# Performance work log

Measured on AMD Instinct MI355X. Metric: run time of the kernel, lower is better.

The kernel has to match this reference:

```python
import jax, jax.numpy as jnp
import numpy as np

IN_DIM, HID, OUT_DIM, PRED_LEN = 33, 64, 2, 25
B, P, T = 1024, 22, 20
EPS = 1e-5


def _lstm_step(Wih, Whh, b, h, c, xt):
    # PyTorch gate order: i, f, g, o
    gates = xt @ Wih.T + h @ Whh.T + b
    i, f, g, o = jnp.split(gates, 4, axis=-1)
    c_new = jax.nn.sigmoid(f) * c + jax.nn.sigmoid(i) * jnp.tanh(g)
    h_new = jax.nn.sigmoid(o) * jnp.tanh(c_new)
    return h_new, c_new


def setup_inputs() -> dict:
    key = jax.random.key(0)
    ks = jax.random.split(key, 20)
    s = 0.1
    inp = {
        "x": jax.random.normal(ks[0], (B, P, T, IN_DIM), dtype=jnp.float32),
        "enc_Wih": jax.random.normal(ks[1], (4 * HID, IN_DIM)) * s,
        "enc_Whh": jax.random.normal(ks[2], (4 * HID, HID)) * s,
        "enc_bih": jax.random.normal(ks[3], (4 * HID,)) * s,
        "enc_bhh": jax.random.normal(ks[4], (4 * HID,)) * s,
        "q_W": jax.random.normal(ks[5], (HID, HID)) * s,
        "q_b": jax.random.normal(ks[6], (HID,)) * s,
        "k_W": jax.random.normal(ks[7], (HID, HID)) * s,
        "k_b": jax.random.normal(ks[8], (HID,)) * s,
        "v_W": jax.random.normal(ks[9], (HID, HID)) * s,
        "v_b": jax.random.normal(ks[10], (HID,)) * s,
        "ln_g": jnp.ones((HID,), jnp.float32),
        "ln_b": jnp.zeros((HID,), jnp.float32),
        "dec_Wih": jax.random.normal(ks[11], (4 * HID, OUT_DIM)) * s,
        "dec_Whh": jax.random.normal(ks[12], (4 * HID, HID)) * s,
        "dec_bih": jax.random.normal(ks[13], (4 * HID,)) * s,
        "dec_bhh": jax.random.normal(ks[14], (4 * HID,)) * s,
        "fc_W": jax.random.normal(ks[15], (OUT_DIM, HID)) * s,
        "fc_b": jax.random.normal(ks[16], (OUT_DIM,)) * s,
    }
    return inp


def reference(x, enc_Wih, enc_Whh, enc_bih, enc_bhh, q_W, q_b, k_W, k_b,
              v_W, v_b, ln_g, ln_b, dec_Wih, dec_Whh, dec_bih, dec_bhh,
              fc_W, fc_b):
    b, p, t, d = x.shape
    n = b * p
    xf = x.reshape(n, t, d)

    # ----- encoder LSTM over history -----
    b_enc = enc_bih + enc_bhh
    def enc_step(carry, xt):
        h, c = carry
        h, c = _lstm_step(enc_Wih, enc_Whh, b_enc, h, c, xt)
        return (h, c), None
    h0 = jnp.zeros((n, HID), x.dtype)
    (hn, cn), _ = jax.lax.scan(enc_step, (h0, h0), xf.transpose(1, 0, 2))

    # ----- interaction GNN (self-attention over players) -----
    last_hidden = hn.reshape(b, p, HID)
    Q = last_hidden @ q_W.T + q_b
    K = last_hidden @ k_W.T + k_b
    V = last_hidden @ v_W.T + v_b
    scores = jnp.einsum('bph,bqh->bpq', Q, K) / jnp.sqrt(jnp.float32(HID))
    attn = jax.nn.softmax(scores, axis=-1)
    ctx = jnp.einsum('bpq,bqh->bph', attn, V)

    # ----- layernorm(residual) -----
    y = last_hidden + ctx
    mu = y.mean(-1, keepdims=True)
    var = y.var(-1, keepdims=True)
    y = (y - mu) / jnp.sqrt(var + EPS) * ln_g + ln_b

    b_dec = dec_bih + dec_bhh
    def dec_step(carry, _):
        h, c, inp = carry
        h, c = _lstm_step(dec_Wih, dec_Whh, b_dec, h, c, inp)
        pred = h @ fc_W.T + fc_b
        return (h, c, pred), pred
    inp0 = xf[:, -1, :OUT_DIM]
    _, preds = jax.lax.scan(dec_step, (y.reshape(n, HID), cn, inp0),
                            None, length=PRED_LEN)  # [PRED_LEN, n, 2]
    return preds.transpose(1, 0, 2).reshape(b, p, PRED_LEN, OUT_DIM)
```

## Files before the change

kernel.cpp:

```cpp
#include <hip/hip_runtime.h>

typedef short short8 __attribute__((ext_vector_type(8)));
typedef float f32x4 __attribute__((ext_vector_type(4)));

#define IN_DIM   33
#define HID      64
#define OUT_DIM  2
#define PRED_LEN 25
#define NB       1024
#define NP       22
#define NT       20
#define EPS      1e-5f

#define SWZ(s,k) (((s) << 7) + ((k) ^ (((s) & 7) << 3)))

__device__ __forceinline__ float fast_rcp(float x){ return __builtin_amdgcn_rcpf(x); }
__device__ __forceinline__ float sigm(float x){ return fast_rcp(1.0f + __expf(-x)); }
__device__ __forceinline__ float tanhf_(float x){ float e = __expf(2.0f*x); return 1.0f - 2.0f*fast_rcp(e + 1.0f); }
__device__ __forceinline__ unsigned short bf_hi(float f){
    unsigned u = __float_as_uint(f);
    return (unsigned short)((u + 0x7fffu + ((u >> 16) & 1u)) >> 16);
}
__device__ __forceinline__ float bf_f(unsigned short h){ return __uint_as_float(((unsigned)h) << 16); }
__device__ __forceinline__ unsigned cvt_pk_bf16(float a, float b){
    unsigned r;
    asm("v_cvt_pk_bf16_f32 %0, %1, %2" : "=v"(r) : "v"(a), "v"(b));
    return r;
}

__global__ __launch_bounds__(256, 2) void nfl_mfma(
    const float* __restrict__ x,
    const float* __restrict__ enc_Wih, const float* __restrict__ enc_Whh,
    const float* __restrict__ enc_bih, const float* __restrict__ enc_bhh,
    const float* __restrict__ q_W, const float* __restrict__ q_b,
    const float* __restrict__ k_W, const float* __restrict__ k_b,
    const float* __restrict__ v_W, const float* __restrict__ v_b,
    const float* __restrict__ ln_g, const float* __restrict__ ln_b,
    const float* __restrict__ dec_Wih, const float* __restrict__ dec_Whh,
    const float* __restrict__ dec_bih, const float* __restrict__ dec_bhh,
    const float* __restrict__ fc_W, const float* __restrict__ fc_b,
    float* __restrict__ out)
{
    __shared__ __align__(16) unsigned char arena[4*8192];
    __shared__ float sh_q [NP*66];
    __shared__ float sh_f [NP*66];
    __shared__ float sh_sc[NP*24];
    __shared__ float sh_p0[32];
    __shared__ float sh_p1[32];
    __shared__ float sh_mu[NP];
    __shared__ float sh_rs[NP];

    float* sh_k = (float*)(arena + 16384);
    float* sh_v = (float*)(arena + 16384 + 8192);

    const int tid  = threadIdx.x;
    const int w    = tid >> 6;
    const int ln   = tid & 63;
    const int lo15 = ln & 15;
    const int qq   = ln >> 4;
    const int jh   = 16*w + lo15;
    const int b    = blockIdx.x;
    const float* xb = x + (size_t)b * NP*NT*IN_DIM;

    auto Ahi = [&](int p){ return (unsigned short*)(arena + p*16384); };
    auto Alo = [&](int p){ return (unsigned short*)(arena + p*16384 + 8192); };

    short8 eBh[4][4], eBl[4][4];
    float bias_e[4];
    #pragma unroll
    for (int nt = 0; nt < 4; nt++){
        int g = 16*w + 64*nt + lo15;
        bias_e[nt] = enc_bih[g] + enc_bhh[g];
        #pragma unroll
        for (int kt = 0; kt < 4; kt++){
            #pragma unroll
            for (int e = 0; e < 8; e++){
                int k = 32*kt + 8*qq + e;
                float v;
                if (k < HID) v = enc_Whh[g*HID + k];
                else { int d = k - HID; v = (d < IN_DIM) ? enc_Wih[g*IN_DIM + d] : 0.0f; }
                unsigned short h = bf_hi(v);
                eBh[nt][kt][e] = (short)h;
                eBl[nt][kt][e] = (short)bf_hi(v - bf_f(h));
            }
        }
    }

    for (int i = tid; i < 4*2048; i += 256) ((unsigned*)arena)[i] = 0;

    float cst[2][4] = {{0,0,0,0},{0,0,0,0}};
    __syncthreads();

    auto nonlin_store = [&](f32x4 (&acc)[2][4], unsigned short* wh,
                            unsigned short* wl, bool save_f){
        #pragma unroll
        for (int m = 0; m < 2; m++){
            #pragma unroll
            for (int jp = 0; jp < 2; jp++){
                const int j0 = 2*jp;
                float hh0, hh1;
                {
                    float gi=acc[m][0][j0], gf=acc[m][1][j0], gg=acc[m][2][j0], go=acc[m][3][j0];
                    float c = sigm(gf)*cst[m][j0] + sigm(gi)*tanhf_(gg);
                    cst[m][j0] = c;
                    hh0 = sigm(go)*tanhf_(c);
                }
                {
                    float gi=acc[m][0][j0+1], gf=acc[m][1][j0+1], gg=acc[m][2][j0+1], go=acc[m][3][j0+1];
                    float c = sigm(gf)*cst[m][j0+1] + sigm(gi)*tanhf_(gg);
                    cst[m][j0+1] = c;
                    hh1 = sigm(go)*tanhf_(c);
                }
                unsigned hp = cvt_pk_bf16(hh0, hh1);
                float r0 = hh0 - __uint_as_float(hp << 16);
                float r1 = hh1 - __uint_as_float(hp & 0xffff0000u);
                unsigned lp = cvt_pk_bf16(r0, r1);
                const int s0 = 16*m + 4*qq + j0;
                if (s0 < NP){
                    int i0 = SWZ(s0, jh);
                    wh[i0] = (unsigned short)hp;
                    wl[i0] = (unsigned short)lp;
                    if (save_f) sh_f[s0*66 + jh] = hh0;
                }
                if (s0 + 1 < NP){
                    int i1 = SWZ(s0 + 1, jh);
                    wh[i1] = (unsigned short)(hp >> 16);
                    wl[i1] = (unsigned short)(lp >> 16);
                    if (save_f) sh_f[(s0+1)*66 + jh] = hh1;
                }
            }
        }
    };

    {
        unsigned short* wh = Ahi(0); unsigned short* wl = Alo(0);
        for (int i = tid; i < NP*IN_DIM; i += 256){
            int s = i / IN_DIM, d = i - s * IN_DIM;
            float v = xb[(s*NT + 0)*IN_DIM + d];
            unsigned short h = bf_hi(v);
            int idx = SWZ(s, HID + d);
            wh[idx] = h; wl[idx] = bf_hi(v - bf_f(h));
        }
    }
    __syncthreads();

    for (int t = 0; t < NT; t++){
        const int p = t & 1;
        unsigned short* rh = Ahi(p);     unsigned short* rl = Alo(p);
        unsigned short* wh = Ahi(1 - p); unsigned short* wl = Alo(1 - p);

        float xr[3];
        const bool have_x = (t + 1 < NT);
        if (have_x){
            #pragma unroll
            for (int sl = 0; sl < 3; sl++){
                int i = tid + 256*sl;
                if (i < NP*IN_DIM){
                    int s = i / IN_DIM, d = i - s * IN_DIM;
                    xr[sl] = xb[(s*NT + (t+1))*IN_DIM + d];
                }
            }
        }

        f32x4 acc[2][4];
        #pragma unroll
        for (int m = 0; m < 2; m++)
            #pragma unroll
            for (int nt = 0; nt < 4; nt++){
                float bb = bias_e[nt];
                acc[m][nt][0]=bb; acc[m][nt][1]=bb; acc[m][nt][2]=bb; acc[m][nt][3]=bb;
            }
        #pragma unroll
        for (int kt = 0; kt < 4; kt++){
            #pragma unroll
            for (int m = 0; m < 2; m++){
                int idx = SWZ(16*m + lo15, 32*kt + 8*qq);
                short8 ah = *reinterpret_cast<const short8*>(&rh[idx]);
                short8 al = *reinterpret_cast<const short8*>(&rl[idx]);
                #pragma unroll
                for (int nt = 0; nt < 4; nt++){
                    acc[m][nt] = __builtin_amdgcn_mfma_f32_16x16x32_bf16(ah, eBh[nt][kt], acc[m][nt], 0,0,0);
                    acc[m][nt] = __builtin_amdgcn_mfma_f32_16x16x32_bf16(al, eBh[nt][kt], acc[m][nt], 0,0,0);
                    acc[m][nt] = __builtin_amdgcn_mfma_f32_16x16x32_bf16(ah, eBl[nt][kt], acc[m][nt], 0,0,0);
                }
            }
        }
        nonlin_store(acc, wh, wl, t == NT-1);
        if (have_x){
            #pragma unroll
            for (int sl = 0; sl < 3; sl++){
                int i = tid + 256*sl;
                if (i < NP*IN_DIM){
                    int s = i / IN_DIM, d = i - s * IN_DIM;
                    unsigned short h = bf_hi(xr[sl]);
                    int idx = SWZ(s, HID + d);
                    wh[idx] = h; wl[idx] = bf_hi(xr[sl] - bf_f(h));
                }
            }
        }
        __syncthreads();
    }

    {
        unsigned short* rh = Ahi(0); unsigned short* rl = Alo(0);
        short8 qBh[3][2], qBl[3][2];
        float qb3[3];
        #pragma unroll
        for (int mat = 0; mat < 3; mat++){
            const float* W  = (mat==0) ? q_W : (mat==1) ? k_W : v_W;
            const float* bb = (mat==0) ? q_b : (mat==1) ? k_b : v_b;
            qb3[mat] = bb[jh];
            #pragma unroll
            for (int kt = 0; kt < 2; kt++){
                #pragma unroll
                for (int e = 0; e < 8; e++){
                    int k = 32*kt + 8*qq + e;
                    float v = W[jh*HID + k];
                    unsigned short h = bf_hi(v);
                    qBh[mat][kt][e] = (short)h;
                    qBl[mat][kt][e] = (short)bf_hi(v - bf_f(h));
                }
            }
        }
        f32x4 qacc[3][2];
        #pragma unroll
        for (int mat = 0; mat < 3; mat++)
            #pragma unroll
            for (int m = 0; m < 2; m++){
                float bb = qb3[mat];
                qacc[mat][m][0]=bb; qacc[mat][m][1]=bb; qacc[mat][m][2]=bb; qacc[mat][m][3]=bb;
            }
        #pragma unroll
        for (int kt = 0; kt < 2; kt++){
            #pragma unroll
            for (int m = 0; m < 2; m++){
                int idx = SWZ(16*m + lo15, 32*kt + 8*qq);
                short8 ah = *reinterpret_cast<const short8*>(&rh[idx]);
                short8 al = *reinterpret_cast<const short8*>(&rl[idx]);
                #pragma unroll
                for (int mat = 0; mat < 3; mat++){
                    qacc[mat][m] = __builtin_amdgcn_mfma_f32_16x16x32_bf16(ah, qBh[mat][kt], qacc[mat][m], 0,0,0);
                    qacc[mat][m] = __builtin_amdgcn_mfma_f32_16x16x32_bf16(al, qBh[mat][kt], qacc[mat][m], 0,0,0);
                    qacc[mat][m] = __builtin_amdgcn_mfma_f32_16x16x32_bf16(ah, qBl[mat][kt], qacc[mat][m], 0,0,0);
                }
            }
        }
        #pragma unroll
        for (int mat = 0; mat < 3; mat++){
            float* dst = (mat==0) ? sh_q : (mat==1) ? sh_k : sh_v;
            #pragma unroll
            for (int m = 0; m < 2; m++)
                #pragma unroll
                for (int j = 0; j < 4; j++){
                    int s = 16*m + 4*qq + j;
                    if (s < NP) dst[s*66 + jh] = qacc[mat][m][j];
                }
        }
    }
    __syncthreads();

    for (int i = tid; i < NP*NP; i += 256){
        int p = i / NP, q = i - p*NP;
        float acc = 0.0f;
        #pragma unroll
        for (int k = 0; k < HID; k++) acc = fmaf(sh_q[p*66 + k], sh_k[q*66 + k], acc);
        sh_sc[p*24 + q] = acc * 0.125f;
    }
    __syncthreads();

    if (tid < NP){
        float m = -1e30f;
        for (int q = 0; q < NP; q++) m = fmaxf(m, sh_sc[tid*24 + q]);
        float sum = 0.0f;
        for (int q = 0; q < NP; q++){ float e = __expf(sh_sc[tid*24 + q] - m); sh_sc[tid*24 + q] = e; sum += e; }
        float inv = fast_rcp(sum);
        for (int q = 0; q < NP; q++) sh_sc[tid*24 + q] *= inv;
    }
    __syncthreads();

    for (int i = tid; i < NP*HID; i += 256){
        int s = i >> 6, j = i & 63;
        float acc = 0.0f;
        #pragma unroll
        for (int q = 0; q < NP; q++) acc = fmaf(sh_sc[s*24 + q], sh_v[q*66 + j], acc);
        sh_f[s*66 + j] += acc;
    }
    __syncthreads();

    if (tid < NP){
        float mu = 0.0f;
        for (int j = 0; j < HID; j++) mu += sh_f[tid*66 + j];
        mu *= (1.0f/HID);
        float var = 0.0f;
        for (int j = 0; j < HID; j++){ float d = sh_f[tid*66 + j] - mu; var += d*d; }
        sh_mu[tid] = mu;
        sh_rs[tid] = rsqrtf(var*(1.0f/HID) + EPS);
    }
    __syncthreads();

    {
        unsigned short* wh = Ahi(0); unsigned short* wl = Alo(0);
        for (int i = tid; i < NP*HID/2; i += 256){
            int s = i >> 5, j0 = (i & 31) << 1;
            float sc = sh_rs[s], mu = sh_mu[s];
            float v0 = (sh_f[s*66 + j0]   - mu) * sc * ln_g[j0]   + ln_b[j0];
            float v1 = (sh_f[s*66 + j0+1] - mu) * sc * ln_g[j0+1] + ln_b[j0+1];
            unsigned hp = cvt_pk_bf16(v0, v1);
            float r0 = v0 - __uint_as_float(hp << 16);
            float r1 = v1 - __uint_as_float(hp & 0xffff0000u);
            unsigned lp = cvt_pk_bf16(r0, r1);
            int idx = SWZ(s, j0);
            *(unsigned*)&wh[idx] = hp;
            *(unsigned*)&wl[idx] = lp;
        }
    }
    if (tid < 32){
        float v0 = 0.0f, v1 = 0.0f;
        if (tid < NP){
            v0 = xb[(tid*NT + NT-1)*IN_DIM + 0];
            v1 = xb[(tid*NT + NT-1)*IN_DIM + 1];
        }
        sh_p0[tid] = v0; sh_p1[tid] = v1;
    }

    short8 dBh[4][2], dBl[4][2];
    float bias_d[4], wd0[4], wd1[4];
    #pragma unroll
    for (int nt = 0; nt < 4; nt++){
        int g = 16*w + 64*nt + lo15;
        bias_d[nt] = dec_bih[g] + dec_bhh[g];
        wd0[nt] = dec_Wih[g*OUT_DIM + 0];
        wd1[nt] = dec_Wih[g*OUT_DIM + 1];
        #pragma unroll
        for (int kt = 0; kt < 2; kt++){
            #pragma unroll
            for (int e = 0; e < 8; e++){
                int k = 32*kt + 8*qq + e;
                float v = dec_Whh[g*HID + k];
                unsigned short h = bf_hi(v);
                dBh[nt][kt][e] = (short)h;
                dBl[nt][kt][e] = (short)bf_hi(v - bf_f(h));
            }
        }
    }
    const int fitem = tid >> 2, fq = tid & 3, fs = fitem >> 1, fo = fitem & 1;
    float fcw[16]; float fcb = 0.0f;
    if (tid < 176){
        #pragma unroll
        for (int jj = 0; jj < 16; jj++) fcw[jj] = fc_W[fo*HID + 16*fq + jj];
        fcb = fc_b[fo];
    }
    float* outb = out + (size_t)b * NP * PRED_LEN * OUT_DIM;
    __syncthreads();

    for (int t = 0; t < PRED_LEN; t++){
        const int p = t & 1;
        unsigned short* rh = Ahi(p);     unsigned short* rl = Alo(p);
        unsigned short* wh = Ahi(1 - p); unsigned short* wl = Alo(1 - p);

        f32x4 acc[2][4];
        #pragma unroll
        for (int m = 0; m < 2; m++){
            #pragma unroll
            for (int j = 0; j < 4; j++){
                int s = 16*m + 4*qq + j;
                float p0 = sh_p0[s], p1 = sh_p1[s];
                #pragma unroll
                for (int nt = 0; nt < 4; nt++)
                    acc[m][nt][j] = bias_d[nt] + wd0[nt]*p0 + wd1[nt]*p1;
            }
        }
        #pragma unroll
        for (int kt = 0; kt < 2; kt++){
            #pragma unroll
            for (int m = 0; m < 2; m++){
                int idx = SWZ(16*m + lo15, 32*kt + 8*qq);
                short8 ah = *reinterpret_cast<const short8*>(&rh[idx]);
                short8 al = *reinterpret_cast<const short8*>(&rl[idx]);
                #pragma unroll
                for (int nt = 0; nt < 4; nt++){
                    acc[m][nt] = __builtin_amdgcn_mfma_f32_16x16x32_bf16(ah, dBh[nt][kt], acc[m][nt], 0,0,0);
                    acc[m][nt] = __builtin_amdgcn_mfma_f32_16x16x32_bf16(al, dBh[nt][kt], acc[m][nt], 0,0,0);
                    acc[m][nt] = __builtin_amdgcn_mfma_f32_16x16x32_bf16(ah, dBl[nt][kt], acc[m][nt], 0,0,0);
                }
            }
        }
        nonlin_store(acc, wh, wl, false);
        __syncthreads();

        if (tid < 176){
            int idx0 = SWZ(fs, 16*fq);
            int idx1 = SWZ(fs, 16*fq + 8);
            short8 h0h = *reinterpret_cast<const short8*>(&wh[idx0]);
            short8 h0l = *reinterpret_cast<const short8*>(&wl[idx0]);
            short8 h1h = *reinterpret_cast<const short8*>(&wh[idx1]);
            short8 h1l = *reinterpret_cast<const short8*>(&wl[idx1]);
            float part = 0.0f;
            #pragma unroll
            for (int e = 0; e < 8; e++){
                part = fmaf(bf_f((unsigned short)h0h[e]) + bf_f((unsigned short)h0l[e]), fcw[e],     part);
                part = fmaf(bf_f((unsigned short)h1h[e]) + bf_f((unsigned short)h1l[e]), fcw[8 + e], part);
            }
            part += __shfl_xor(part, 1);
            part += __shfl_xor(part, 2);
            if (fq == 0){
                float pred = part + fcb;
                outb[(fs*PRED_LEN + t)*OUT_DIM + fo] = pred;
                if (fo == 0) sh_p0[fs] = pred; else sh_p1[fs] = pred;
            }
        }
        __syncthreads();
    }
}

extern "C" void kernel_launch(void* const* d_in, const int* in_sizes, int n_in,
                              void* d_out, int out_size, void* d_ws, size_t ws_size,
                              hipStream_t stream) {
    const float* x        = (const float*)d_in[0];
    const float* enc_Wih  = (const float*)d_in[1];
    const float* enc_Whh  = (const float*)d_in[2];
    const float* enc_bih  = (const float*)d_in[3];
    const float* enc_bhh  = (const float*)d_in[4];
    const float* q_W      = (const float*)d_in[5];
    const float* q_b      = (const float*)d_in[6];
    const float* k_W      = (const float*)d_in[7];
    const float* k_b      = (const float*)d_in[8];
    const float* v_W      = (const float*)d_in[9];
    const float* v_b      = (const float*)d_in[10];
    const float* ln_g     = (const float*)d_in[11];
    const float* ln_b     = (const float*)d_in[12];
    const float* dec_Wih  = (const float*)d_in[13];
    const float* dec_Whh  = (const float*)d_in[14];
    const float* dec_bih  = (const float*)d_in[15];
    const float* dec_bhh  = (const float*)d_in[16];
    const float* fc_W     = (const float*)d_in[17];
    const float* fc_b     = (const float*)d_in[18];
    float* out = (float*)d_out;

    nfl_mfma<<<dim3(NB), dim3(256), 0, stream>>>(
        x, enc_Wih, enc_Whh, enc_bih, enc_bhh,
        q_W, q_b, k_W, k_b, v_W, v_b, ln_g, ln_b,
        dec_Wih, dec_Whh, dec_bih, dec_bhh, fc_W, fc_b, out);
}
```

Before: 359.7 us.

## Process two batch groups per block to fill MFMA row tiles

Each block now handles two batches (44 player rows padded to 48) instead of one, using three 16-row MFMA tiles rather than two. The old layout wasted 10 of 32 padded rows, and the new one wastes 4 of 48, so more useful work is done per LSTM step and per barrier. Weight fragments loaded into registers are also shared across twice the rows. The grid is halved to 512 blocks. Shared memory is reorganised to fit, with attention scores, layernorm stats and decoder inputs packed into unused parts of the arena. The trade-offs are more registers, fewer blocks to fill the 256 CUs, and extra index arithmetic.

Measured after the change: 339.6 us. 5.6% less time.

```diff
diff --git a/kernel.cpp b/kernel.cpp
--- a/kernel.cpp
+++ b/kernel.cpp
@@ -11,6 +11,7 @@
 #define NP       22
 #define NT       20
 #define EPS      1e-5f
+#define QSTR     65
 
 #define SWZ(s,k) (((s) << 7) + ((k) ^ (((s) & 7) << 3)))
 
@@ -41,17 +42,12 @@
     const float* __restrict__ fc_W, const float* __restrict__ fc_b,
     float* __restrict__ out)
 {
-    __shared__ __align__(16) unsigned char arena[4*8192];
-    __shared__ float sh_q [NP*66];
-    __shared__ float sh_f [NP*66];
-    __shared__ float sh_sc[NP*24];
-    __shared__ float sh_p0[32];
-    __shared__ float sh_p1[32];
-    __shared__ float sh_mu[NP];
-    __shared__ float sh_rs[NP];
-
-    float* sh_k = (float*)(arena + 16384);
-    float* sh_v = (float*)(arena + 16384 + 8192);
+    __shared__ __align__(16) unsigned char arena[2*24576];
+    __shared__ float sh_q[44*QSTR];
+
+    float* arena_f = (float*)arena;
+    float* sh_k = (float*)(arena + 24576);
+    float* sh_v = sh_k + 44*QSTR;
 
     const int tid  = threadIdx.x;
     const int w    = tid >> 6;
@@ -59,11 +55,12 @@
     const int lo15 = ln & 15;
     const int qq   = ln >> 4;
     const int jh   = 16*w + lo15;
-    const int b    = blockIdx.x;
-    const float* xb = x + (size_t)b * NP*NT*IN_DIM;
-
-    auto Ahi = [&](int p){ return (unsigned short*)(arena + p*16384); };
-    auto Alo = [&](int p){ return (unsigned short*)(arena + p*16384 + 8192); };
+    const int bid  = blockIdx.x;
+    const float* xb0 = x + (size_t)(2*bid) * NP*NT*IN_DIM;
+    const float* xb1 = xb0 + NP*NT*IN_DIM;
+
+    auto Ahi = [&](int p){ return (unsigned short*)(arena + p*24576); };
+    auto Alo = [&](int p){ return (unsigned short*)(arena + p*24576 + 12288); };
 
     short8 eBh[4][4], eBl[4][4];
     float bias_e[4];
@@ -86,61 +83,86 @@
         }
     }
 
-    for (int i = tid; i < 4*2048; i += 256) ((unsigned*)arena)[i] = 0;
-
-    float cst[2][4] = {{0,0,0,0},{0,0,0,0}};
-    __syncthreads();
-
-    auto nonlin_store = [&](f32x4 (&acc)[2][4], unsigned short* wh,
-                            unsigned short* wl, bool save_f){
-        #pragma unroll
-        for (int m = 0; m < 2; m++){
+    for (int i = tid; i < 12288; i += 256) ((unsigned*)arena)[i] = 0;
+
+    float cst[3][4];
+    #pragma unroll
+    for (int mt = 0; mt < 3; mt++)
+        #pragma unroll
+        for (int j = 0; j < 4; j++) cst[mt][j] = 0.0f;
+    __syncthreads();
+
+    auto stage_x_regs = [&](int t, float (&xr)[6]){
+        #pragma unroll
+        for (int sl = 0; sl < 6; sl++){
+            int i = tid + 256*sl;
+            if (i < 2*NP*IN_DIM){
+                int bb = (i >= NP*IN_DIM);
+                int rem = i - bb*NP*IN_DIM;
+                int s = rem / IN_DIM, d = rem - s*IN_DIM;
+                const float* xb = bb ? xb1 : xb0;
+                xr[sl] = xb[(s*NT + t)*IN_DIM + d];
+            }
+        }
+    };
+    auto stage_x_write = [&](float (&xr)[6], unsigned short* wh, unsigned short* wl){
+        #pragma unroll
+        for (int sl = 0; sl < 6; sl++){
+            int i = tid + 256*sl;
+            if (i < 2*NP*IN_DIM){
+                int bb = (i >= NP*IN_DIM);
+                int rem = i - bb*NP*IN_DIM;
+                int s = rem / IN_DIM, d = rem - s*IN_DIM;
+                unsigned short h = bf_hi(xr[sl]);
+                int idx = SWZ(bb*24 + s, HID + d);
+                wh[idx] = h; wl[idx] = bf_hi(xr[sl] - bf_f(h));
+            }
+        }
+    };
+
+    auto nonlin_store = [&](f32x4 (&acc)[3][4], unsigned short* wh, unsigned short* wl){
+        #pragma unroll
+        for (int mt = 0; mt < 3; mt++){
             #pragma unroll
             for (int jp = 0; jp < 2; jp++){
                 const int j0 = 2*jp;
                 float hh0, hh1;
                 {
-                    float gi=acc[m][0][j0], gf=acc[m][1][j0], gg=acc[m][2][j0], go=acc[m][3][j0];
-                    float c = sigm(gf)*cst[m][j0] + sigm(gi)*tanhf_(gg);
-                    cst[m][j0] = c;
+                    float gi=acc[mt][0][j0], gf=acc[mt][1][j0], gg=acc[mt][2][j0], go=acc[mt][3][j0];
+                    float c = sigm(gf)*cst[mt][j0] + sigm(gi)*tanhf_(gg);
+                    cst[mt][j0] = c;
                     hh0 = sigm(go)*tanhf_(c);
                 }
                 {
-                    float gi=acc[m][0][j0+1], gf=acc[m][1][j0+1], gg=acc[m][2][j0+1], go=acc[m][3][j0+1];
-                    float c = sigm(gf)*cst[m][j0+1] + sigm(gi)*tanhf_(gg);
-                    cst[m][j0+1] = c;
+                    float gi=acc[mt][0][j0+1], gf=acc[mt][1][j0+1], gg=acc[mt][2][j0+1], go=acc[mt][3][j0+1];
+                    float c = sigm(gf)*cst[mt][j0+1] + sigm(gi)*tanhf_(gg);
+                    cst[mt][j0+1] = c;
                     hh1 = sigm(go)*tanhf_(c);
                 }
                 unsigned hp = cvt_pk_bf16(hh0, hh1);
                 float r0 = hh0 - __uint_as_float(hp << 16);
                 float r1 = hh1 - __uint_as_float(hp & 0xffff0000u);
                 unsigned lp = cvt_pk_bf16(r0, r1);
-                const int s0 = 16*m + 4*qq + j0;
-                if (s0 < NP){
+                const int s0 = 16*mt + 4*qq + j0;
+                const int ps0 = s0 - ((s0 >= 24) ? 24 : 0);
+                if (ps0 < NP){
                     int i0 = SWZ(s0, jh);
                     wh[i0] = (unsigned short)hp;
                     wl[i0] = (unsigned short)lp;
-                    if (save_f) sh_f[s0*66 + jh] = hh0;
-                }
-                if (s0 + 1 < NP){
+                }
+                if (ps0 + 1 < NP){
                     int i1 = SWZ(s0 + 1, jh);
                     wh[i1] = (unsigned short)(hp >> 16);
                     wl[i1] = (unsigned short)(lp >> 16);
-                    if (save_f) sh_f[(s0+1)*66 + jh] = hh1;
                 }
             }
         }
     };
 
     {
-        unsigned short* wh = Ahi(0); unsigned short* wl = Alo(0);
-        for (int i = tid; i < NP*IN_DIM; i += 256){
-            int s = i / IN_DIM, d = i - s * IN_DIM;
-            float v = xb[(s*NT + 0)*IN_DIM + d];
-            unsigned short h = bf_hi(v);
-            int idx = SWZ(s, HID + d);
-            wh[idx] = h; wl[idx] = bf_hi(v - bf_f(h));
-        }
+        float xr[6];
+        stage_x_regs(0, xr);
+        stage_x_write(xr, Ahi(0), Alo(0));
     }
     __syncthreads();
 
@@ -149,55 +171,35 @@
         unsigned short* rh = Ahi(p);     unsigned short* rl = Alo(p);
         unsigned short* wh = Ahi(1 - p); unsigned short* wl = Alo(1 - p);
 
-        float xr[3];
+        float xr[6];
         const bool have_x = (t + 1 < NT);
-        if (have_x){
-            #pragma unroll
-            for (int sl = 0; sl < 3; sl++){
-                int i = tid + 256*sl;
-                if (i < NP*IN_DIM){
-                    int s = i / IN_DIM, d = i - s * IN_DIM;
-                    xr[sl] = xb[(s*NT + (t+1))*IN_DIM + d];
-                }
-            }
-        }
-
-        f32x4 acc[2][4];
-        #pragma unroll
-        for (int m = 0; m < 2; m++)
+        if (have_x) stage_x_regs(t + 1, xr);
+
+        f32x4 acc[3][4];
+        #pragma unroll
+        for (int mt = 0; mt < 3; mt++)
             #pragma unroll
             for (int nt = 0; nt < 4; nt++){
                 float bb = bias_e[nt];
-                acc[m][nt][0]=bb; acc[m][nt][1]=bb; acc[m][nt][2]=bb; acc[m][nt][3]=bb;
+                acc[mt][nt][0]=bb; acc[mt][nt][1]=bb; acc[mt][nt][2]=bb; acc[mt][nt][3]=bb;
             }
         #pragma unroll
         for (int kt = 0; kt < 4; kt++){
             #pragma unroll
-            for (int m = 0; m < 2; m++){
-                int idx = SWZ(16*m + lo15, 32*kt + 8*qq);
+            for (int mt = 0; mt < 3; mt++){
+                int idx = SWZ(16*mt + lo15, 32*kt + 8*qq);
                 short8 ah = *reinterpret_cast<const short8*>(&rh[idx]);
                 short8 al = *reinterpret_cast<const short8*>(&rl[idx]);
                 #pragma unroll
                 for (int nt = 0; nt < 4; nt++){
-                    acc[m][nt] = __builtin_amdgcn_mfma_f32_16x16x32_bf16(ah, eBh[nt][kt], acc[m][nt], 0,0,0);
-                    acc[m][nt] = __builtin_amdgcn_mfma_f32_16x16x32_bf16(al, eBh[nt][kt], acc[m][nt], 0,0,0);
-                    acc[m][nt] = __builtin_amdgcn_mfma_f32_16x16x32_bf16(ah, eBl[nt][kt], acc[m][nt], 0,0,0);
-                }
-            }
-        }
-        nonlin_store(acc, wh, wl, t == NT-1);
-        if (have_x){
-            #pragma unroll
-            for (int sl = 0; sl < 3; sl++){
-                int i = tid + 256*sl;
-                if (i < NP*IN_DIM){
-                    int s = i / IN_DIM, d = i - s * IN_DIM;
-                    unsigned short h = bf_hi(xr[sl]);
-                    int idx = SWZ(s, HID + d);
-                    wh[idx] = h; wl[idx] = bf_hi(xr[sl] - bf_f(h));
-                }
-            }
-        }
+                    acc[mt][nt] = __builtin_amdgcn_mfma_f32_16x16x32_bf16(ah, eBh[nt][kt], acc[mt][nt], 0,0,0);
+                    acc[mt][nt] = __builtin_amdgcn_mfma_f32_16x16x32_bf16(al, eBh[nt][kt], acc[mt][nt], 0,0,0);
+                    acc[mt][nt] = __builtin_amdgcn_mfma_f32_16x16x32_bf16(ah, eBl[nt][kt], acc[mt][nt], 0,0,0);
+                }
+            }
+        }
+        nonlin_store(acc, wh, wl);
+        if (have_x) stage_x_write(xr, wh, wl);
         __syncthreads();
     }
 
@@ -222,26 +224,26 @@
                 }
             }
         }
-        f32x4 qacc[3][2];
+        f32x4 qacc[3][3];
         #pragma unroll
         for (int mat = 0; mat < 3; mat++)
             #pragma unroll
-            for (int m = 0; m < 2; m++){
+            for (int mt = 0; mt < 3; mt++){
                 float bb = qb3[mat];
-                qacc[mat][m][0]=bb; qacc[mat][m][1]=bb; qacc[mat][m][2]=bb; qacc[mat][m][3]=bb;
+                qacc[mat][mt][0]=bb; qacc[mat][mt][1]=bb; qacc[mat][mt][2]=bb; qacc[mat][mt][3]=bb;
             }
         #pragma unroll
         for (int kt = 0; kt < 2; kt++){
             #pragma unroll
-            for (int m = 0; m < 2; m++){
-                int idx = SWZ(16*m + lo15, 32*kt + 8*qq);
+            for (int mt = 0; mt < 3; mt++){
+                int idx = SWZ(16*mt + lo15, 32*kt + 8*qq);
                 short8 ah = *reinterpret_cast<const short8*>(&rh[idx]);
                 short8 al = *reinterpret_cast<const short8*>(&rl[idx]);
                 #pragma unroll
                 for (int mat = 0; mat < 3; mat++){
-                    qacc[mat][m] = __builtin_amdgcn_mfma_f32_16x16x32_bf16(ah, qBh[mat][kt], qacc[mat][m], 0,0,0);
-                    qacc[mat][m] = __builtin_amdgcn_mfma_f32_16x16x32_bf16(al, qBh[mat][kt], qacc[mat][m], 0,0,0);
-                    qacc[mat][m] = __builtin_amdgcn_mfma_f32_16x16x32_bf16(ah, qBl[mat][kt], qacc[mat][m], 0,0,0);
+                    qacc[mat][mt] = __builtin_amdgcn_mfma_f32_16x16x32_bf16(ah, qBh[mat][kt], qacc[mat][mt], 0,0,0);
+                    qacc[mat][mt] = __builtin_amdgcn_mfma_f32_16x16x32_bf16(al, qBh[mat][kt], qacc[mat][mt], 0,0,0);
+                    qacc[mat][mt] = __builtin_amdgcn_mfma_f32_16x16x32_bf16(ah, qBl[mat][kt], qacc[mat][mt], 0,0,0);
                 }
             }
         }
@@ -249,78 +251,107 @@
         for (int mat = 0; mat < 3; mat++){
             float* dst = (mat==0) ? sh_q : (mat==1) ? sh_k : sh_v;
             #pragma unroll
-            for (int m = 0; m < 2; m++)
+            for (int mt = 0; mt < 3; mt++)
                 #pragma unroll
                 for (int j = 0; j < 4; j++){
-                    int s = 16*m + 4*qq + j;
-                    if (s < NP) dst[s*66 + jh] = qacc[mat][m][j];
-                }
-        }
-    }
-    __syncthreads();
-
-    for (int i = tid; i < NP*NP; i += 256){
-        int p = i / NP, q = i - p*NP;
+                    int s = 16*mt + 4*qq + j;
+                    int bb = (s >= 24) ? 1 : 0;
+                    int ps = s - 24*bb;
+                    if (ps < NP) dst[(bb*NP + ps)*QSTR + jh] = qacc[mat][mt][j];
+                }
+        }
+    }
+    __syncthreads();
+
+    for (int i = tid; i < 2*NP*NP; i += 256){
+        int bb = (i >= NP*NP);
+        int rem = i - bb*NP*NP;
+        int p = rem / NP, q = rem - p*NP;
         float acc = 0.0f;
         #pragma unroll
-        for (int k = 0; k < HID; k++) acc = fmaf(sh_q[p*66 + k], sh_k[q*66 + k], acc);
-        sh_sc[p*24 + q] = acc * 0.125f;
-    }
-    __syncthreads();
-
-    if (tid < NP){
+        for (int k = 0; k < HID; k++)
+            acc = fmaf(sh_q[(bb*NP + p)*QSTR + k], sh_k[(bb*NP + q)*QSTR + k], acc);
+        arena_f[(bb*24 + p)*64 + 32 + q] = acc * 0.125f;
+    }
+    __syncthreads();
+
+    if (tid < 2*NP){
+        int bb = (tid >= NP);
+        int p = tid - bb*NP;
+        float* row = arena_f + (bb*24 + p)*64 + 32;
         float m = -1e30f;
-        for (int q = 0; q < NP; q++) m = fmaxf(m, sh_sc[tid*24 + q]);
+        for (int q = 0; q < NP; q++) m = fmaxf(m, row[q]);
         float sum = 0.0f;
-        for (int q = 0; q < NP; q++){ float e = __expf(sh_sc[tid*24 + q] - m); sh_sc[tid*24 + q] = e; sum += e; }
+        for (int q = 0; q < NP; q++){ float e = __expf(row[q] - m); row[q] = e; sum += e; }
         float inv = fast_rcp(sum);
-        for (int q = 0; q < NP; q++) sh_sc[tid*24 + q] *= inv;
-    }
-    __syncthreads();
-
-    for (int i = tid; i < NP*HID; i += 256){
-        int s = i >> 6, j = i & 63;
-        float acc = 0.0f;
-        #pragma unroll
-        for (int q = 0; q < NP; q++) acc = fmaf(sh_sc[s*24 + q], sh_v[q*66 + j], acc);
-        sh_f[s*66 + j] += acc;
-    }
-    __syncthreads();
-
-    if (tid < NP){
+        for (int q = 0; q < NP; q++) row[q] *= inv;
+    }
+    __syncthreads();
+
+    {
+        unsigned short* h0 = Ahi(0); unsigned short* l0 = Alo(0);
+        for (int i = tid; i < 2*NP*HID; i += 256){
+            int bb = (i >= NP*HID);
+            int rem = i - bb*NP*HID;
+            int ps = rem >> 6, j = rem & 63;
+            int r = bb*24 + ps;
+            const float* sc = arena_f + r*64 + 32;
+            float acc = 0.0f;
+            #pragma unroll
+            for (int q = 0; q < NP; q++) acc = fmaf(sc[q], sh_v[(bb*NP + q)*QSTR + j], acc);
+            int idx = SWZ(r, j);
+            float h = bf_f(h0[idx]) + bf_f(l0[idx]);
+            sh_q[(bb*NP + ps)*QSTR + j] = h + acc;
+        }
+    }
+    __syncthreads();
+
+    if (tid < 2*NP){
+        int bb = (tid >= NP);
+        int ps = tid - bb*NP;
+        const float* yrow = sh_q + (bb*NP + ps)*QSTR;
         float mu = 0.0f;
-        for (int j = 0; j < HID; j++) mu += sh_f[tid*66 + j];
+        for (int j = 0; j < HID; j++) mu += yrow[j];
         mu *= (1.0f/HID);
         float var = 0.0f;
-        for (int j = 0; j < HID; j++){ float d = sh_f[tid*66 + j] - mu; var += d*d; }
-        sh_mu[tid] = mu;
-        sh_rs[tid] = rsqrtf(var*(1.0f/HID) + EPS);
+        for (int j = 0; j < HID; j++){ float d = yrow[j] - mu; var += d*d; }
+        arena_f[(bb*24 + ps)*64 + 32 + 22] = mu;
+        arena_f[(bb*24 + ps)*64 + 32 + 23] = rsqrtf(var*(1.0f/HID) + EPS);
     }
     __syncthreads();
 
     {
         unsigned short* wh = Ahi(0); unsigned short* wl = Alo(0);
-        for (int i = tid; i < NP*HID/2; i += 256){
-            int s = i >> 5, j0 = (i & 31) << 1;
-            float sc = sh_rs[s], mu = sh_mu[s];
-            float v0 = (sh_f[s*66 + j0]   - mu) * sc * ln_g[j0]   + ln_b[j0];
-            float v1 = (sh_f[s*66 + j0+1] - mu) * sc * ln_g[j0+1] + ln_b[j0+1];
+        for (int i = tid; i < 2*NP*HID/2; i += 256){
+            int bb = (i >= NP*HID/2);
+            int rem = i - bb*NP*HID/2;
+            int ps = rem >> 5, j0 = (rem & 31) << 1;
+            int r = bb*24 + ps;
+            float mu = arena_f[r*64 + 32 + 22];
+            float sc = arena_f[r*64 + 32 + 23];
+            const float* yrow = sh_q + (bb*NP + ps)*QSTR;
+            float v0 = (yrow[j0]   - mu) * sc * ln_g[j0]   + ln_b[j0];
+            float v1 = (yrow[j0+1] - mu) * sc * ln_g[j0+1] + ln_b[j0+1];
             unsigned hp = cvt_pk_bf16(v0, v1);
             float r0 = v0 - __uint_as_float(hp << 16);
             float r1 = v1 - __uint_as_float(hp & 0xffff0000u);
             unsigned lp = cvt_pk_bf16(r0, r1);
-            int idx = SWZ(s, j0);
+            int idx = SWZ(r, j0);
             *(unsigned*)&wh[idx] = hp;
             *(unsigned*)&wl[idx] = lp;
         }
     }
-    if (tid < 32){
+    if (tid < 48){
+        int bb = (tid >= 24);
+        int ps = tid - 24*bb;
         float v0 = 0.0f, v1 = 0.0f;
-        if (tid < NP){
-            v0 = xb[(tid*NT + NT-1)*IN_DIM + 0];
-            v1 = xb[(tid*NT + NT-1)*IN_DIM + 1];
-        }
-        sh_p0[tid] = v0; sh_p1[tid] = v1;
+        if (ps < NP){
+            const float* xb = bb ? xb1 : xb0;
+            v0 = xb[(ps*NT + NT-1)*IN_DIM + 0];
+            v1 = xb[(ps*NT + NT-1)*IN_DIM + 1];
+        }
+        arena_f[6144 + tid*64 + 32] = v0;
+        arena_f[6144 + tid*64 + 33] = v1;
     }
 
     short8 dBh[4][2], dBl[4][2];
@@ -343,14 +374,16 @@
             }
         }
     }
-    const int fitem = tid >> 2, fq = tid & 3, fs = fitem >> 1, fo = fitem & 1;
-    float fcw[16]; float fcb = 0.0f;
+    const int fitem = tid >> 1, fq = tid & 1;
+    const int fbb = fitem / 44, frem = fitem - fbb*44, fs = frem >> 1, fo = frem & 1;
+    float fcw[32]; float fcb = 0.0f;
     if (tid < 176){
         #pragma unroll
-        for (int jj = 0; jj < 16; jj++) fcw[jj] = fc_W[fo*HID + 16*fq + jj];
+        for (int jj = 0; jj < 32; jj++) fcw[jj] = fc_W[fo*HID + 32*fq + jj];
         fcb = fc_b[fo];
     }
-    float* outb = out + (size_t)b * NP * PRED_LEN * OUT_DIM;
+    float* outb0 = out + (size_t)(2*bid) * NP * PRED_LEN * OUT_DIM;
+    float* outb1 = outb0 + NP * PRED_LEN * OUT_DIM;
     __syncthreads();
 
     for (int t = 0; t < PRED_LEN; t++){
@@ -358,55 +391,56 @@
         unsigned short* rh = Ahi(p);     unsigned short* rl = Alo(p);
         unsigned short* wh = Ahi(1 - p); unsigned short* wl = Alo(1 - p);
 
-        f32x4 acc[2][4];
-        #pragma unroll
-        for (int m = 0; m < 2; m++){
+        f32x4 acc[3][4];
+        #pragma unroll
+        for (int mt = 0; mt < 3; mt++){
             #pragma unroll
             for (int j = 0; j < 4; j++){
-                int s = 16*m + 4*qq + j;
-                float p0 = sh_p0[s], p1 = sh_p1[s];
+                int s = 16*mt + 4*qq + j;
+                float p0 = arena_f[6144 + s*64 + 32];
+                float p1 = arena_f[6144 + s*64 + 33];
                 #pragma unroll
                 for (int nt = 0; nt < 4; nt++)
-                    acc[m][nt][j] = bias_d[nt] + wd0[nt]*p0 + wd1[nt]*p1;
+                    acc[mt][nt][j] = bias_d[nt] + wd0[nt]*p0 + wd1[nt]*p1;
             }
         }
         #pragma unroll
         for (int kt = 0; kt < 2; kt++){
             #pragma unroll
-            for (int m = 0; m < 2; m++){
-                int idx = SWZ(16*m + lo15, 32*kt + 8*qq);
+            for (int mt = 0; mt < 3; mt++){
+                int idx = SWZ(16*mt + lo15, 32*kt + 8*qq);
                 short8 ah = *reinterpret_cast<const short8*>(&rh[idx]);
                 short8 al = *reinterpret_cast<const short8*>(&rl[idx]);
                 #pragma unroll
                 for (int nt = 0; nt < 4; nt++){
-                    acc[m][nt] = __builtin_amdgcn_mfma_f32_16x16x32_bf16(ah, dBh[nt][kt], acc[m][nt], 0,0,0);
-                    acc[m][nt] = __builtin_amdgcn_mfma_f32_16x16x32_bf16(al, dBh[nt][kt], acc[m][nt], 0,0,0);
-                    acc[m][nt] = __builtin_amdgcn_mfma_f32_16x16x32_bf16(ah, dBl[nt][kt], acc[m][nt], 0,0,0);
-                }
-            }
-        }
-        nonlin_store(acc, wh, wl, false);
+                    acc[mt][nt] = __builtin_amdgcn_mfma_f32_16x16x32_bf16(ah, dBh[nt][kt], acc[mt][nt], 0,0,0);
+                    acc[mt][nt] = __builtin_amdgcn_mfma_f32_16x16x32_bf16(al, dBh[nt][kt], acc[mt][nt], 0,0,0);
+                    acc[mt][nt] = __builtin_amdgcn_mfma_f32_16x16x32_bf16(ah, dBl[nt][kt], acc[mt][nt], 0,0,0);
+                }
+            }
+        }
+        nonlin_store(acc, wh, wl);
         __syncthreads();
 
         if (tid < 176){
-            int idx0 = SWZ(fs, 16*fq);
-            int idx1 = SWZ(fs, 16*fq + 8);
-            short8 h0h = *reinterpret_cast<const short8*>(&wh[idx0]);
-            short8 h0l = *reinterpret_cast<const short8*>(&wl[idx0]);
-            short8 h1h = *reinterpret_cast<const short8*>(&wh[idx1]);
-            short8 h1l = *reinterpret_cast<const short8*>(&wl[idx1]);
+            const int row = fbb*24 + fs;
             float part = 0.0f;
             #pragma unroll
-            for (int e = 0; e < 8; e++){
-                part = fmaf(bf_f((unsigned short)h0h[e]) + bf_f((unsigned short)h0l[e]), fcw[e],     part);
-                part = fmaf(bf_f((unsigned short)h1h[e]) + bf_f((unsigned short)h1l[e]), fcw[8 + e], part);
+            for (int e4 = 0; e4 < 4; e4++){
+                int idx = SWZ(row, 32*fq + 8*e4);
+                short8 hh = *reinterpret_cast<const short8*>(&wh[idx]);
+                short8 ll = *reinterpret_cast<const short8*>(&wl[idx]);
+                #pragma unroll
+                for (int e = 0; e < 8; e++)
+                    part = fmaf(bf_f((unsigned short)hh[e]) + bf_f((unsigned short)ll[e]),
+                                fcw[8*e4 + e], part);
             }
             part += __shfl_xor(part, 1);
-            part += __shfl_xor(part, 2);
             if (fq == 0){
                 float pred = part + fcb;
+                float* outb = fbb ? outb1 : outb0;
                 outb[(fs*PRED_LEN + t)*OUT_DIM + fo] = pred;
-                if (fo == 0) sh_p0[fs] = pred; else sh_p1[fs] = pred;
+                arena_f[6144 + (fbb*24 + fs)*64 + 32 + fo] = pred;
             }
         }
         __syncthreads();
@@ -437,7 +471,7 @@
     const float* fc_b     = (const float*)d_in[18];
     float* out = (float*)d_out;
 
-    nfl_mfma<<<dim3(NB), dim3(256), 0, stream>>>(
+    nfl_mfma<<<dim3(NB/2), dim3(256), 0, stream>>>(
         x, enc_Wih, enc_Whh, enc_bih, enc_bhh,
         q_W, q_b, k_W, k_b, v_W, v_b, ln_g, ln_b,
         dec_Wih, dec_Whh, dec_bih, dec_bhh, fc_W, fc_b, out);
```
